# Optimization experiments

Hardware: AMD Instinct MI355X
Metric: run time of the kernel (lower is better)

The kernel has to match this reference:

```python
import math
import jax, jax.numpy as jnp
import numpy as np

# Module config (init_kwargs)
GRID = (11, 16, 24)          # (T, H, W) latent grid, T odd so T-1 == 2*(T//2)
POOL = 128                   # pool_size / block size
SPARSITY = 0.9
TXT_LEN = 384                # txt_len, txt_first=False
HEADS, HDIM = 8, 128
FFL = GRID[1] * GRID[2]      # first_frame_len = H*W = 384
SEQ = GRID[0] * FFL + TXT_LEN  # 4608 tokens, 36 blocks of 128


def _rearr(t):
    # rearrange_with_remaining, h%8==0 and w%8==0 path.
    # t: [b, (f h w), n, d] with f = T-1 frames (first frame excluded)
    b, s, n, d = t.shape
    T, H, W = GRID
    fn, hn, wn = T // 2, H // 8, W // 8
    x = t.transpose(0, 2, 1, 3).reshape(b * n, fn, 2, hn, 8, wn, 8, d)
    # 'b (fn fb)(hn hb)(wn wb) d -> b (fn hn wn fb hb wb) d'
    x = x.transpose(0, 1, 3, 5, 2, 4, 6, 7).reshape(b * n, s, d)
    return x.reshape(b, n, s, d).transpose(0, 2, 1, 3)


def _inv_rearr(t):
    b, s, n, d = t.shape
    T, H, W = GRID
    fn, hn, wn = T // 2, H // 8, W // 8
    x = t.transpose(0, 2, 1, 3).reshape(b * n, fn, hn, wn, 2, 8, 8, d)
    x = x.transpose(0, 1, 4, 2, 5, 3, 6, 7).reshape(b * n, s, d)
    return x.reshape(b, n, s, d).transpose(0, 2, 1, 3)


def _avgpool(t):
    # seq divisible by POOL -> mean over each block (tail branch unused)
    b, s, n, d = t.shape
    return t.reshape(b, s // POOL, POOL, n, d).mean(axis=2)


def _forward(q, k, v):
    b, s, n, d = q.shape
    scale = jnp.asarray(d, q.dtype) ** -0.5
    # do_tensor_rearrange_pooling on concatenated qkv (txt_first=False)
    qkv = jnp.concatenate([q, k, v], axis=0)
    f_part = qkv[:, :FFL]
    i_part = qkv[:, FFL:s - TXT_LEN]
    t_part = qkv[:, s - TXT_LEN:]
    qkv2 = jnp.concatenate([_rearr(i_part), f_part, t_part], axis=1)
    pool = _avgpool(qkv2)
    q2, k2, v2 = jnp.split(qkv2, 3, axis=0)
    qp, kp, _ = jnp.split(pool, 3, axis=0)
    # pooled block scores + softmax
    ps = jax.nn.softmax(jnp.einsum('blnd,bsnd->bnls', qp, kp) * scale, axis=-1)
    nb = s // POOL
    keep = math.ceil(nb * (1.0 - SPARSITY))
    thr = jax.lax.top_k(ps, keep)[0][..., -1:]
    mask = ps >= thr                              # [B, n, nb, nb] bool
    prot = (FFL + TXT_LEN + POOL - 1) // POOL
    mask = mask.at[:, :, -prot:, :].set(True)
    mask = mask.at[:, :, :, -prot:].set(True)
    bm = mask[0]                                  # [n, nb, nb] per-head block mask (batch 0, as kernel uses)
    tok = jnp.repeat(jnp.repeat(bm, POOL, axis=1), POOL, axis=2)  # [n, S, S]
    # block-sparse attention == masked dense attention over selected kv blocks
    scores = jnp.einsum('bqnd,bknd->bnqk', q2, k2) * scale
    scores = jnp.where(tok[None], scores, jnp.asarray(-1e30, scores.dtype))
    p = jax.nn.softmax(scores, axis=-1)
    x = jnp.einsum('bnqk,bknd->bqnd', p, v2)
    # do_tensor_inv_rearrange (txt_first=False: concat(f, i, t))
    si = s - TXT_LEN - FFL
    xi = _inv_rearr(x[:, :si])
    xf = x[:, si:si + FFL]
    xt = x[:, si + FFL:]
    return jnp.concatenate([xf, xi, xt], axis=1)


def setup_inputs() -> dict:
    key = jax.random.key(0)
    kq, kk, kv = jax.random.split(key, 3)
    q = jax.random.normal(kq, (1, SEQ, HEADS, HDIM), dtype=jnp.float32)
    k = jax.random.normal(kk, (1, SEQ, HEADS, HDIM), dtype=jnp.float32)
    v = jax.random.normal(kv, (1, SEQ, HEADS, HDIM), dtype=jnp.float32)
    t_b_idx = jnp.arange(2, dtype=jnp.int64 if jax.config.jax_enable_x64 else jnp.int32)
    return {'q': q, 'k': k, 'v': v, 't_b_idx': t_b_idx}


def reference(q, k, v, t_b_idx):
    # t_idx = t_b_idx[0] = 0, skip_timesteps = 0 -> sparse branch (static)
    return _forward(q, k, v)
```

## Files before the change

### kernel.cpp

```cpp
#include <hip/hip_runtime.h>


typedef __attribute__((ext_vector_type(8))) _Float16 half8;
typedef __attribute__((ext_vector_type(4))) _Float16 half4;
typedef __attribute__((ext_vector_type(2))) _Float16 half2v;
typedef __attribute__((ext_vector_type(4))) float float4v;

#define KROW 136
#define VROW 72
#define VSROW 138
#define PPROW 40

__device__ __forceinline__ int orig_pos(int j) {
    if (j >= 3840) return (j < 4224) ? (j - 3840) : j;
    int blk = j >> 7;
    int r   = j & 127;
    int f   = blk / 6;
    int rem = blk - f * 6;
    int b2  = rem / 3;
    int e   = rem - b2 * 3;
    int a   = r >> 6;
    int c   = (r >> 3) & 7;
    int g   = r & 7;
    return 384 + (f * 2 + a) * 384 + (b2 * 8 + c) * 24 + e * 8 + g;
}

__device__ __forceinline__ void cp16(const void* g, void* l) {
    __builtin_amdgcn_global_load_lds((const __attribute__((address_space(1))) void*)g,
                                     (__attribute__((address_space(3))) void*)l, 16, 0, 0);
}

__global__ __launch_bounds__(256) void conv_kernel(const float* __restrict__ k,
                                                   const float* __restrict__ v,
                                                   short* __restrict__ Kc,
                                                   unsigned* __restrict__ Vt32,
                                                   float* __restrict__ kpart) {
    __shared__ __align__(16) short KsL[64 * KROW];
    __shared__ short VsL[64 * VSROW];
    __shared__ float Rs[32 * 128];
    int bx  = blockIdx.x;
    int tid = threadIdx.x;
    int sub = bx & 1;
    int kb  = (bx >> 1) % 36;
    int h   = bx / 72;

    int lr  = tid >> 3;
    int ld4 = (tid & 7) << 2;

    float ksum[16];
#pragma unroll
    for (int i = 0; i < 16; ++i) ksum[i] = 0.f;

#pragma unroll
    for (int pass = 0; pass < 2; ++pass) {
        int lt  = pass * 32 + lr;
        int tok = sub * 64 + lt;
        int op  = orig_pos(kb * 128 + tok);
        const float* kr = k + ((size_t)op * 8 + h) * 128;
        const float* vr = v + ((size_t)op * 8 + h) * 128;
#pragma unroll
        for (int j = 0; j < 4; ++j) {
            int d = ld4 + j * 32;
            float4v xk = *reinterpret_cast<const float4v*>(kr + d);
            float4v xv = *reinterpret_cast<const float4v*>(vr + d);
            half4 hk;
            half2v hv0, hv1;
#pragma unroll
            for (int i = 0; i < 4; ++i) { hk[i] = (_Float16)xk[i]; ksum[j * 4 + i] += xk[i]; }
            hv0[0] = (_Float16)xv[0]; hv0[1] = (_Float16)xv[1];
            hv1[0] = (_Float16)xv[2]; hv1[1] = (_Float16)xv[3];
            *reinterpret_cast<half4*>(&KsL[lt * KROW + d]) = hk;
            *reinterpret_cast<half2v*>(&VsL[lt * VSROW + d]) = hv0;
            *reinterpret_cast<half2v*>(&VsL[lt * VSROW + d + 2]) = hv1;
        }
    }
#pragma unroll
    for (int j = 0; j < 4; ++j)
#pragma unroll
        for (int i = 0; i < 4; ++i)
            Rs[lr * 128 + ld4 + j * 32 + i] = ksum[j * 4 + i];
    __syncthreads();

    {
        const float4v* src = reinterpret_cast<const float4v*>(KsL);
        float4v* dst = reinterpret_cast<float4v*>(Kc + ((size_t)((h * 36 + kb) * 128) + sub * 64) * KROW);
        for (int i = tid; i < 1088; i += 256) dst[i] = src[i];
    }

    {
        const unsigned short* Vsu = (const unsigned short*)VsL;
        unsigned* vo = Vt32 + (size_t)((h * 36 + kb) * 2 + sub) * 128 * (VROW / 2);
#pragma unroll
        for (int it = 0; it < 16; ++it) {
            int i   = it * 256 + tid;
            int tw  = i & 31;
            int dim = i >> 5;
            unsigned lo = Vsu[(2 * tw) * VSROW + dim];
            unsigned hi = Vsu[(2 * tw + 1) * VSROW + dim];
            vo[dim * (VROW / 2) + tw] = (hi << 16) | lo;
        }
    }

    if (tid < 128) {
        float s = 0.f;
#pragma unroll
        for (int g = 0; g < 32; ++g) s += Rs[g * 128 + tid];
        kpart[(size_t)((h * 36 + kb) * 2 + sub) * 128 + tid] = s;
    }
}

__global__ __launch_bounds__(256) void poolq_kernel(const float* __restrict__ q,
                                                    float* __restrict__ qp) {
    __shared__ float Rs[8 * 128];
    int bx  = blockIdx.x;
    int tid = threadIdx.x;
    int kb  = bx % 36;
    int h   = bx / 36;

    int dq = (tid & 31) << 2;
    int g  = tid >> 5;
    float4v acc = {0.f, 0.f, 0.f, 0.f};
#pragma unroll
    for (int it = 0; it < 16; ++it) {
        int t  = g + it * 8;
        int op = orig_pos(kb * 128 + t);
        float4v x = *reinterpret_cast<const float4v*>(q + ((size_t)op * 8 + h) * 128 + dq);
        acc[0] += x[0]; acc[1] += x[1]; acc[2] += x[2]; acc[3] += x[3];
    }
#pragma unroll
    for (int i = 0; i < 4; ++i) Rs[g * 128 + dq + i] = acc[i];
    __syncthreads();

    if (tid < 128) {
        float s = 0.f;
#pragma unroll
        for (int g2 = 0; g2 < 8; ++g2) s += Rs[g2 * 128 + tid];
        qp[(h * 36 + kb) * 128 + tid] = s;
    }
}

__global__ __launch_bounds__(256, 3) void flash_kernel(const float* __restrict__ q,
                                                       const short* __restrict__ Kc,
                                                       const short* __restrict__ Vt,
                                                       const float* __restrict__ qp,
                                                       const float* __restrict__ kpart,
                                                       float* __restrict__ out,
                                                       float* __restrict__ pO,
                                                       float* __restrict__ pL) {
    __shared__ __align__(16) short Ks[64 * KROW];
    __shared__ __align__(16) short Vsh[128 * VROW];
    __shared__ __align__(16) short Ph[4 * 32 * PPROW];
    __shared__ int Ls[40];
    __shared__ float Lf[64];

    int t = blockIdx.x;
    int h, qb, half, nkb = 0, kbase = 0, pidx = -1;
    if (t < 288) {
        h = t & 7;
        int rest = t >> 3;
        int qbh = rest / 6, r2 = rest % 6;
        half = r2 / 3;
        int chunk = r2 % 3;
        qb = 30 + qbh; nkb = 12; kbase = chunk * 12; pidx = t;
    } else {
        int t2 = t - 288;
        h = t2 & 7;
        int rest = t2 >> 3;
        qb = rest >> 1; half = rest & 1;
    }

    int tid = threadIdx.x, wave = tid >> 6, lane = tid & 63;
    int m16 = lane & 15, quad = lane >> 4;
    int rh = wave & 1, th = wave >> 1;

    constexpr float kScale = 0.08838834764831845f * 1.4426950408889634f;

    half8 aq[2][4];
#pragma unroll
    for (int rg = 0; rg < 2; ++rg) {
        int qrow_frag = qb * 128 + half * 64 + rh * 32 + rg * 16 + m16;
        const float* qrp = q + ((size_t)orig_pos(qrow_frag) * 8 + h) * 128;
#pragma unroll
        for (int kc = 0; kc < 4; ++kc) {
            float4v x0 = *reinterpret_cast<const float4v*>(qrp + kc * 32 + quad * 8);
            float4v x1 = *reinterpret_cast<const float4v*>(qrp + kc * 32 + quad * 8 + 4);
#pragma unroll
            for (int j = 0; j < 4; ++j) {
                aq[rg][kc][j]     = (_Float16)(x0[j] * kScale);
                aq[rg][kc][4 + j] = (_Float16)(x1[j] * kScale);
            }
        }
    }

    if (pidx < 0 && wave == 0) {
        float s = -1e30f;
        if (lane < 36) {
            const float4v* qv  = (const float4v*)(qp + (h * 36 + qb) * 128);
            const float4v* kv0 = (const float4v*)(kpart + (size_t)((h * 36 + lane) * 2) * 128);
            const float4v* kv1 = kv0 + 32;
            float acc = 0.f;
            for (int i = 0; i < 32; ++i) {
                float4v a = qv[i], b0 = kv0[i], b1 = kv1[i];
                acc += a[0] * (b0[0] + b1[0]) + a[1] * (b0[1] + b1[1])
                     + a[2] * (b0[2] + b1[2]) + a[3] * (b0[3] + b1[3]);
            }
            s = acc;
        }
        float tmp = s;
        float thr = 0.f;
        for (int i = 0; i < 4; ++i) {
            float mx = tmp;
            for (int off = 1; off < 64; off <<= 1) mx = fmaxf(mx, __shfl_xor(mx, off));
            thr = mx;
            unsigned long long bal = __ballot(tmp == mx);
            int low = __ffsll(bal) - 1;
            if (lane == low) tmp = -3e38f;
        }
        bool keep = (lane < 36) && ((s >= thr) || (lane >= 30));
        unsigned long long mk = __ballot(keep);
        if (lane == 0) Ls[0] = __popcll(mk);
        if (keep) {
            int pos = __popcll(mk & ((1ull << lane) - 1ull));
            Ls[1 + pos] = lane;
        }
    }
    __syncthreads();
    if (pidx < 0) nkb = Ls[0];

    float l_r[2][4];
    float4v o[2][8];
#pragma unroll
    for (int rg = 0; rg < 2; ++rg) {
#pragma unroll
        for (int r = 0; r < 4; ++r) l_r[rg][r] = 0.f;
#pragma unroll
        for (int dt = 0; dt < 8; ++dt) { o[rg][dt][0] = 0.f; o[rg][dt][1] = 0.f; o[rg][dt][2] = 0.f; o[rg][dt][3] = 0.f; }
    }

    short* Phw = Ph + wave * (32 * PPROW);

    int ntile = nkb * 2;
    for (int it = 0; it < ntile; ++it) {
        int kb  = (pidx >= 0) ? (kbase + (it >> 1)) : Ls[1 + (it >> 1)];
        int sub = it & 1;
        const char* gK = (const char*)(Kc + ((size_t)((h * 36 + kb) * 128) + sub * 64) * KROW);
        const char* gV = (const char*)(Vt + (size_t)((h * 36 + kb) * 2 + sub) * 128 * VROW);

        __syncthreads();
        {
            char* lK = (char*)Ks;
            char* lV = (char*)Vsh;
            int off = lane * 16;
            for (int c = wave; c < 35; c += 4) {
                if (c < 17) cp16(gK + c * 1024 + off, lK + c * 1024 + off);
                else        cp16(gV + (c - 17) * 1024 + off, lV + (c - 17) * 1024 + off);
            }
        }
        __syncthreads();

        float4v sacc[2][2];
#pragma unroll
        for (int rg = 0; rg < 2; ++rg)
#pragma unroll
            for (int nt = 0; nt < 2; ++nt) { sacc[rg][nt][0] = 0.f; sacc[rg][nt][1] = 0.f; sacc[rg][nt][2] = 0.f; sacc[rg][nt][3] = 0.f; }
#pragma unroll
        for (int nt = 0; nt < 2; ++nt)
#pragma unroll
            for (int kc = 0; kc < 4; ++kc) {
                half8 bk = *reinterpret_cast<const half8*>(&Ks[(th * 32 + nt * 16 + m16) * KROW + kc * 32 + quad * 8]);
                sacc[0][nt] = __builtin_amdgcn_mfma_f32_16x16x32_f16(aq[0][kc], bk, sacc[0][nt], 0, 0, 0);
                sacc[1][nt] = __builtin_amdgcn_mfma_f32_16x16x32_f16(aq[1][kc], bk, sacc[1][nt], 0, 0, 0);
            }

#pragma unroll
        for (int rg = 0; rg < 2; ++rg)
#pragma unroll
            for (int r = 0; r < 4; ++r) {
                float p0 = exp2f(sacc[rg][0][r]);
                float p1 = exp2f(sacc[rg][1][r]);
                sacc[rg][0][r] = p0; sacc[rg][1][r] = p1;
                l_r[rg][r] += p0 + p1;
            }

#pragma unroll
        for (int rg = 0; rg < 2; ++rg)
#pragma unroll
            for (int nt = 0; nt < 2; ++nt)
#pragma unroll
                for (int r = 0; r < 4; ++r) {
                    union { _Float16 hf; short s; } cv;
                    cv.hf = (_Float16)sacc[rg][nt][r];
                    Phw[(rg * 16 + quad * 4 + r) * PPROW + nt * 16 + m16] = cv.s;
                }
        half8 ap[2];
#pragma unroll
        for (int rg = 0; rg < 2; ++rg)
            ap[rg] = *reinterpret_cast<const half8*>(&Phw[(rg * 16 + m16) * PPROW + quad * 8]);

#pragma unroll
        for (int dt = 0; dt < 8; ++dt) {
            half8 bv = *reinterpret_cast<const half8*>(&Vsh[(dt * 16 + m16) * VROW + th * 32 + quad * 8]);
            o[0][dt] = __builtin_amdgcn_mfma_f32_16x16x32_f16(ap[0], bv, o[0][dt], 0, 0, 0);
            o[1][dt] = __builtin_amdgcn_mfma_f32_16x16x32_f16(ap[1], bv, o[1][dt], 0, 0, 0);
        }
    }

#pragma unroll
    for (int rg = 0; rg < 2; ++rg)
#pragma unroll
        for (int r = 0; r < 4; ++r)
            for (int sh = 1; sh < 16; sh <<= 1) l_r[rg][r] += __shfl_xor(l_r[rg][r], sh);

    __syncthreads();
    {
        float* red = rh ? (float*)Vsh : (float*)Ks;
        if (th == 1) {
#pragma unroll
            for (int rg = 0; rg < 2; ++rg) {
#pragma unroll
                for (int dt = 0; dt < 8; ++dt)
#pragma unroll
                    for (int r = 0; r < 4; ++r)
                        red[(rg * 16 + quad * 4 + r) * 132 + dt * 16 + m16] = o[rg][dt][r];
                if (m16 == 0)
#pragma unroll
                    for (int r = 0; r < 4; ++r)
                        Lf[rh * 32 + rg * 16 + quad * 4 + r] = l_r[rg][r];
            }
        }
        __syncthreads();
        if (th == 0) {
#pragma unroll
            for (int rg = 0; rg < 2; ++rg)
#pragma unroll
                for (int dt = 0; dt < 8; ++dt)
#pragma unroll
                    for (int r = 0; r < 4; ++r)
                        o[rg][dt][r] += red[(rg * 16 + quad * 4 + r) * 132 + dt * 16 + m16];

            if (pidx >= 0) {
                float* po = pO + (size_t)pidx * 8192;
#pragma unroll
                for (int rg = 0; rg < 2; ++rg)
#pragma unroll
                    for (int r = 0; r < 4; ++r) {
                        int row = rh * 32 + rg * 16 + quad * 4 + r;
                        float lt2 = l_r[rg][r] + Lf[row];
#pragma unroll
                        for (int dt = 0; dt < 8; ++dt)
                            po[row * 128 + dt * 16 + m16] = o[rg][dt][r];
                        if (m16 == 0) pL[pidx * 64 + row] = lt2;
                    }
            } else {
#pragma unroll
                for (int rg = 0; rg < 2; ++rg)
#pragma unroll
                    for (int r = 0; r < 4; ++r) {
                        int row = rh * 32 + rg * 16 + quad * 4 + r;
                        int qrow = qb * 128 + half * 64 + row;
                        size_t base = ((size_t)orig_pos(qrow) * 8 + h) * 128;
                        float inv = 1.f / (l_r[rg][r] + Lf[row]);
#pragma unroll
                        for (int dt = 0; dt < 8; ++dt)
                            out[base + dt * 16 + m16] = o[rg][dt][r] * inv;
                    }
            }
        }
    }
}

__global__ void combine_kernel(const float* __restrict__ pO, const float* __restrict__ pL,
                               float* __restrict__ out) {
    int gb = blockIdx.x;
    int g  = gb >> 3;
    int rg = gb & 7;
    int h    = g / 12;
    int rem  = g % 12;
    int qbh  = rem >> 1;
    int half = rem & 1;
    int qb   = 30 + qbh;
    int base_t = (qbh * 6 + half * 3) * 8 + h;

    int tid = threadIdx.x;
    int d   = tid & 127;
    int r0  = tid >> 7;
#pragma unroll
    for (int itr = 0; itr < 4; ++itr) {
        int row = rg * 8 + r0 + itr * 2;
        float l = pL[(base_t + 0) * 64 + row] + pL[(base_t + 8) * 64 + row] + pL[(base_t + 16) * 64 + row];
        float acc = pO[(size_t)(base_t + 0) * 8192 + row * 128 + d]
                  + pO[(size_t)(base_t + 8) * 8192 + row * 128 + d]
                  + pO[(size_t)(base_t + 16) * 8192 + row * 128 + d];
        int qrow = qb * 128 + half * 64 + row;
        out[((size_t)orig_pos(qrow) * 8 + h) * 128 + d] = acc / l;
    }
}

extern "C" void kernel_launch(void* const* d_in, const int* in_sizes, int n_in,
                              void* d_out, int out_size, void* d_ws, size_t ws_size,
                              hipStream_t stream) {
    const float* q = (const float*)d_in[0];
    const float* k = (const float*)d_in[1];
    const float* v = (const float*)d_in[2];
    float* out = (float*)d_out;

    char* w = (char*)d_ws;
    short* Kc    = (short*)(w);
    short* Vt    = (short*)(w + 10027008);
    float* qp    = (float*)(w + 20643840);
    float* kpart = (float*)(w + 20791296);
    float* pL    = (float*)(w + 21086208);
    float* pO    = (float*)(w + 21159936);

    conv_kernel<<<dim3(576), dim3(256), 0, stream>>>(k, v, Kc, (unsigned*)Vt, kpart);
    poolq_kernel<<<dim3(288), dim3(256), 0, stream>>>(q, qp);
    flash_kernel<<<dim3(768), dim3(256), 0, stream>>>(q, Kc, Vt, qp, kpart, out, pO, pL);
    combine_kernel<<<dim3(768), dim3(256), 0, stream>>>(pO, pL, out);
}
```

Baseline: 172.4 us.

## Merge prep kernels and fold split-K combine into flash via atomic tickets

Merges the K/V conversion and Q pooling kernels into a single prep launch. It also removes the separate combine kernel: each split-K flash block takes an atomic ticket, and the last of the three blocks in a group reduces the partial outputs and writes the final result. This removes two kernel launches and the gaps between them. In exchange, the reduction runs serialized inside one block per group, and correctness depends on threadfence ordering and on the ticket array being zeroed in the prep kernel.

```diff
diff --git a/kernel.cpp b/kernel.cpp
--- a/kernel.cpp
+++ b/kernel.cpp
@@ -30,112 +30,115 @@
                                      (__attribute__((address_space(3))) void*)l, 16, 0, 0);
 }
 
-__global__ __launch_bounds__(256) void conv_kernel(const float* __restrict__ k,
+__global__ __launch_bounds__(256) void prep_kernel(const float* __restrict__ q,
+                                                   const float* __restrict__ k,
                                                    const float* __restrict__ v,
                                                    short* __restrict__ Kc,
                                                    unsigned* __restrict__ Vt32,
-                                                   float* __restrict__ kpart) {
+                                                   float* __restrict__ qp,
+                                                   float* __restrict__ kpart,
+                                                   int* __restrict__ tickets) {
     __shared__ __align__(16) short KsL[64 * KROW];
     __shared__ short VsL[64 * VSROW];
     __shared__ float Rs[32 * 128];
     int bx  = blockIdx.x;
     int tid = threadIdx.x;
-    int sub = bx & 1;
-    int kb  = (bx >> 1) % 36;
-    int h   = bx / 72;
-
-    int lr  = tid >> 3;
-    int ld4 = (tid & 7) << 2;
-
-    float ksum[16];
-#pragma unroll
-    for (int i = 0; i < 16; ++i) ksum[i] = 0.f;
-
-#pragma unroll
-    for (int pass = 0; pass < 2; ++pass) {
-        int lt  = pass * 32 + lr;
-        int tok = sub * 64 + lt;
-        int op  = orig_pos(kb * 128 + tok);
-        const float* kr = k + ((size_t)op * 8 + h) * 128;
-        const float* vr = v + ((size_t)op * 8 + h) * 128;
-#pragma unroll
-        for (int j = 0; j < 4; ++j) {
-            int d = ld4 + j * 32;
-            float4v xk = *reinterpret_cast<const float4v*>(kr + d);
-            float4v xv = *reinterpret_cast<const float4v*>(vr + d);
-            half4 hk;
-            half2v hv0, hv1;
-#pragma unroll
-            for (int i = 0; i < 4; ++i) { hk[i] = (_Float16)xk[i]; ksum[j * 4 + i] += xk[i]; }
-            hv0[0] = (_Float16)xv[0]; hv0[1] = (_Float16)xv[1];
-            hv1[0] = (_Float16)xv[2]; hv1[1] = (_Float16)xv[3];
-            *reinterpret_cast<half4*>(&KsL[lt * KROW + d]) = hk;
-            *reinterpret_cast<half2v*>(&VsL[lt * VSROW + d]) = hv0;
-            *reinterpret_cast<half2v*>(&VsL[lt * VSROW + d + 2]) = hv1;
-        }
-    }
-#pragma unroll
-    for (int j = 0; j < 4; ++j)
-#pragma unroll
-        for (int i = 0; i < 4; ++i)
-            Rs[lr * 128 + ld4 + j * 32 + i] = ksum[j * 4 + i];
-    __syncthreads();
-
-    {
-        const float4v* src = reinterpret_cast<const float4v*>(KsL);
-        float4v* dst = reinterpret_cast<float4v*>(Kc + ((size_t)((h * 36 + kb) * 128) + sub * 64) * KROW);
-        for (int i = tid; i < 1088; i += 256) dst[i] = src[i];
-    }
-
-    {
-        const unsigned short* Vsu = (const unsigned short*)VsL;
-        unsigned* vo = Vt32 + (size_t)((h * 36 + kb) * 2 + sub) * 128 * (VROW / 2);
+
+    if (bx < 576) {
+        int sub = bx & 1;
+        int kb  = (bx >> 1) % 36;
+        int h   = bx / 72;
+
+        int lr  = tid >> 3;
+        int ld4 = (tid & 7) << 2;
+
+        float ksum[16];
+#pragma unroll
+        for (int i = 0; i < 16; ++i) ksum[i] = 0.f;
+
+#pragma unroll
+        for (int pass = 0; pass < 2; ++pass) {
+            int lt  = pass * 32 + lr;
+            int tok = sub * 64 + lt;
+            int op  = orig_pos(kb * 128 + tok);
+            const float* kr = k + ((size_t)op * 8 + h) * 128;
+            const float* vr = v + ((size_t)op * 8 + h) * 128;
+#pragma unroll
+            for (int j = 0; j < 4; ++j) {
+                int d = ld4 + j * 32;
+                float4v xk = *reinterpret_cast<const float4v*>(kr + d);
+                float4v xv = *reinterpret_cast<const float4v*>(vr + d);
+                half4 hk;
+                half2v hv0, hv1;
+#pragma unroll
+                for (int i = 0; i < 4; ++i) { hk[i] = (_Float16)xk[i]; ksum[j * 4 + i] += xk[i]; }
+                hv0[0] = (_Float16)xv[0]; hv0[1] = (_Float16)xv[1];
+                hv1[0] = (_Float16)xv[2]; hv1[1] = (_Float16)xv[3];
+                *reinterpret_cast<half4*>(&KsL[lt * KROW + d]) = hk;
+                *reinterpret_cast<half2v*>(&VsL[lt * VSROW + d]) = hv0;
+                *reinterpret_cast<half2v*>(&VsL[lt * VSROW + d + 2]) = hv1;
+            }
+        }
+#pragma unroll
+        for (int j = 0; j < 4; ++j)
+#pragma unroll
+            for (int i = 0; i < 4; ++i)
+                Rs[lr * 128 + ld4 + j * 32 + i] = ksum[j * 4 + i];
+        __syncthreads();
+
+        {
+            const float4v* src = reinterpret_cast<const float4v*>(KsL);
+            float4v* dst = reinterpret_cast<float4v*>(Kc + ((size_t)((h * 36 + kb) * 128) + sub * 64) * KROW);
+            for (int i = tid; i < 1088; i += 256) dst[i] = src[i];
+        }
+
+        {
+            const unsigned short* Vsu = (const unsigned short*)VsL;
+            unsigned* vo = Vt32 + (size_t)((h * 36 + kb) * 2 + sub) * 128 * (VROW / 2);
+#pragma unroll
+            for (int it = 0; it < 16; ++it) {
+                int i   = it * 256 + tid;
+                int tw  = i & 31;
+                int dim = i >> 5;
+                unsigned lo = Vsu[(2 * tw) * VSROW + dim];
+                unsigned hi = Vsu[(2 * tw + 1) * VSROW + dim];
+                vo[dim * (VROW / 2) + tw] = (hi << 16) | lo;
+            }
+        }
+
+        if (tid < 128) {
+            float s = 0.f;
+#pragma unroll
+            for (int g = 0; g < 32; ++g) s += Rs[g * 128 + tid];
+            kpart[(size_t)((h * 36 + kb) * 2 + sub) * 128 + tid] = s;
+        }
+    } else {
+        int bx2 = bx - 576;
+        int kb  = bx2 % 36;
+        int h   = bx2 / 36;
+
+        if (bx2 == 0 && tid < 96) tickets[tid] = 0;
+
+        int dq = (tid & 31) << 2;
+        int g  = tid >> 5;
+        float4v acc = {0.f, 0.f, 0.f, 0.f};
 #pragma unroll
         for (int it = 0; it < 16; ++it) {
-            int i   = it * 256 + tid;
-            int tw  = i & 31;
-            int dim = i >> 5;
-            unsigned lo = Vsu[(2 * tw) * VSROW + dim];
-            unsigned hi = Vsu[(2 * tw + 1) * VSROW + dim];
-            vo[dim * (VROW / 2) + tw] = (hi << 16) | lo;
-        }
-    }
-
-    if (tid < 128) {
-        float s = 0.f;
-#pragma unroll
-        for (int g = 0; g < 32; ++g) s += Rs[g * 128 + tid];
-        kpart[(size_t)((h * 36 + kb) * 2 + sub) * 128 + tid] = s;
-    }
-}
-
-__global__ __launch_bounds__(256) void poolq_kernel(const float* __restrict__ q,
-                                                    float* __restrict__ qp) {
-    __shared__ float Rs[8 * 128];
-    int bx  = blockIdx.x;
-    int tid = threadIdx.x;
-    int kb  = bx % 36;
-    int h   = bx / 36;
-
-    int dq = (tid & 31) << 2;
-    int g  = tid >> 5;
-    float4v acc = {0.f, 0.f, 0.f, 0.f};
-#pragma unroll
-    for (int it = 0; it < 16; ++it) {
-        int t  = g + it * 8;
-        int op = orig_pos(kb * 128 + t);
-        float4v x = *reinterpret_cast<const float4v*>(q + ((size_t)op * 8 + h) * 128 + dq);
-        acc[0] += x[0]; acc[1] += x[1]; acc[2] += x[2]; acc[3] += x[3];
-    }
-#pragma unroll
-    for (int i = 0; i < 4; ++i) Rs[g * 128 + dq + i] = acc[i];
-    __syncthreads();
-
-    if (tid < 128) {
-        float s = 0.f;
-#pragma unroll
-        for (int g2 = 0; g2 < 8; ++g2) s += Rs[g2 * 128 + tid];
-        qp[(h * 36 + kb) * 128 + tid] = s;
+            int t  = g + it * 8;
+            int op = orig_pos(kb * 128 + t);
+            float4v x = *reinterpret_cast<const float4v*>(q + ((size_t)op * 8 + h) * 128 + dq);
+            acc[0] += x[0]; acc[1] += x[1]; acc[2] += x[2]; acc[3] += x[3];
+        }
+#pragma unroll
+        for (int i = 0; i < 4; ++i) Rs[g * 128 + dq + i] = acc[i];
+        __syncthreads();
+
+        if (tid < 128) {
+            float s = 0.f;
+#pragma unroll
+            for (int g2 = 0; g2 < 8; ++g2) s += Rs[g2 * 128 + tid];
+            qp[(h * 36 + kb) * 128 + tid] = s;
+        }
     }
 }
 
@@ -146,7 +149,8 @@
                                                        const float* __restrict__ kpart,
                                                        float* __restrict__ out,
                                                        float* __restrict__ pO,
-                                                       float* __restrict__ pL) {
+                                                       float* __restrict__ pL,
+                                                       int* __restrict__ tickets) {
     __shared__ __align__(16) short Ks[64 * KROW];
     __shared__ __align__(16) short Vsh[128 * VROW];
     __shared__ __align__(16) short Ph[4 * 32 * PPROW];
@@ -154,11 +158,12 @@
     __shared__ float Lf[64];
 
     int t = blockIdx.x;
-    int h, qb, half, nkb = 0, kbase = 0, pidx = -1;
+    int h, qb, half, nkb = 0, kbase = 0, pidx = -1, qbh = 0;
     if (t < 288) {
         h = t & 7;
         int rest = t >> 3;
-        int qbh = rest / 6, r2 = rest % 6;
+        qbh = rest / 6;
+        int r2 = rest % 6;
         half = r2 / 3;
         int chunk = r2 % 3;
         qb = 30 + qbh; nkb = 12; kbase = chunk * 12; pidx = t;
@@ -367,32 +372,29 @@
             }
         }
     }
-}
-
-__global__ void combine_kernel(const float* __restrict__ pO, const float* __restrict__ pL,
-                               float* __restrict__ out) {
-    int gb = blockIdx.x;
-    int g  = gb >> 3;
-    int rg = gb & 7;
-    int h    = g / 12;
-    int rem  = g % 12;
-    int qbh  = rem >> 1;
-    int half = rem & 1;
-    int qb   = 30 + qbh;
-    int base_t = (qbh * 6 + half * 3) * 8 + h;
-
-    int tid = threadIdx.x;
-    int d   = tid & 127;
-    int r0  = tid >> 7;
-#pragma unroll
-    for (int itr = 0; itr < 4; ++itr) {
-        int row = rg * 8 + r0 + itr * 2;
-        float l = pL[(base_t + 0) * 64 + row] + pL[(base_t + 8) * 64 + row] + pL[(base_t + 16) * 64 + row];
-        float acc = pO[(size_t)(base_t + 0) * 8192 + row * 128 + d]
-                  + pO[(size_t)(base_t + 8) * 8192 + row * 128 + d]
-                  + pO[(size_t)(base_t + 16) * 8192 + row * 128 + d];
-        int qrow = qb * 128 + half * 64 + row;
-        out[((size_t)orig_pos(qrow) * 8 + h) * 128 + d] = acc / l;
+
+    if (pidx >= 0) {
+        int grp = h * 12 + qbh * 2 + half;
+        __threadfence();
+        __syncthreads();
+        if (tid == 0) Ls[39] = atomicAdd(&tickets[grp], 1);
+        __syncthreads();
+        if (Ls[39] == 2) {
+            __threadfence();
+            int base_t = (qbh * 6 + half * 3) * 8 + h;
+            int d  = tid & 127;
+            int r0 = tid >> 7;
+#pragma unroll 4
+            for (int itr = 0; itr < 32; ++itr) {
+                int row = r0 + itr * 2;
+                float l = pL[(base_t + 0) * 64 + row] + pL[(base_t + 8) * 64 + row] + pL[(base_t + 16) * 64 + row];
+                float acc = pO[(size_t)(base_t + 0) * 8192 + row * 128 + d]
+                          + pO[(size_t)(base_t + 8) * 8192 + row * 128 + d]
+                          + pO[(size_t)(base_t + 16) * 8192 + row * 128 + d];
+                int qrow = qb * 128 + half * 64 + row;
+                out[((size_t)orig_pos(qrow) * 8 + h) * 128 + d] = acc / l;
+            }
+        }
     }
 }
 
@@ -411,9 +413,8 @@
     float* kpart = (float*)(w + 20791296);
     float* pL    = (float*)(w + 21086208);
     float* pO    = (float*)(w + 21159936);
-
-    conv_kernel<<<dim3(576), dim3(256), 0, stream>>>(k, v, Kc, (unsigned*)Vt, kpart);
-    poolq_kernel<<<dim3(288), dim3(256), 0, stream>>>(q, qp);
-    flash_kernel<<<dim3(768), dim3(256), 0, stream>>>(q, Kc, Vt, qp, kpart, out, pO, pL);
-    combine_kernel<<<dim3(768), dim3(256), 0, stream>>>(pO, pL, out);
+    int*   tick  = (int*)(w + 30597120);
+
+    prep_kernel<<<dim3(864), dim3(256), 0, stream>>>(q, k, v, Kc, (unsigned*)Vt, qp, kpart, tick);
+    flash_kernel<<<dim3(768), dim3(256), 0, stream>>>(q, Kc, Vt, qp, kpart, out, pO, pL, tick);
 }
```

Measured after the change: 215.3 us. 24.8% more time.

## Merge prep kernels, split heavy query blocks four ways, reuse K LDS for P

Applied to the files above, without the earlier changes.

Merges the K/V conversion and Q pooling kernels into one launch. The dense protected query blocks are now split into four KV chunks of 9 blocks instead of three of 12, and the grid is remapped to 864 blocks that interleave heavy and light work items. The P staging buffer now aliases the K shared tile, which needs an extra barrier per tile but frees LDS, and launch bounds are raised to 4 blocks per SM. The aim is better load balance and occupancy plus one fewer launch, at the cost of an extra sync and more partial outputs for the combine step to read.

```diff
diff --git a/kernel.cpp b/kernel.cpp
--- a/kernel.cpp
+++ b/kernel.cpp
@@ -30,116 +30,116 @@
                                      (__attribute__((address_space(3))) void*)l, 16, 0, 0);
 }
 
-__global__ __launch_bounds__(256) void conv_kernel(const float* __restrict__ k,
+__global__ __launch_bounds__(256) void prep_kernel(const float* __restrict__ q,
+                                                   const float* __restrict__ k,
                                                    const float* __restrict__ v,
                                                    short* __restrict__ Kc,
                                                    unsigned* __restrict__ Vt32,
+                                                   float* __restrict__ qp,
                                                    float* __restrict__ kpart) {
     __shared__ __align__(16) short KsL[64 * KROW];
     __shared__ short VsL[64 * VSROW];
     __shared__ float Rs[32 * 128];
     int bx  = blockIdx.x;
     int tid = threadIdx.x;
-    int sub = bx & 1;
-    int kb  = (bx >> 1) % 36;
-    int h   = bx / 72;
-
-    int lr  = tid >> 3;
-    int ld4 = (tid & 7) << 2;
-
-    float ksum[16];
-#pragma unroll
-    for (int i = 0; i < 16; ++i) ksum[i] = 0.f;
-
-#pragma unroll
-    for (int pass = 0; pass < 2; ++pass) {
-        int lt  = pass * 32 + lr;
-        int tok = sub * 64 + lt;
-        int op  = orig_pos(kb * 128 + tok);
-        const float* kr = k + ((size_t)op * 8 + h) * 128;
-        const float* vr = v + ((size_t)op * 8 + h) * 128;
-#pragma unroll
-        for (int j = 0; j < 4; ++j) {
-            int d = ld4 + j * 32;
-            float4v xk = *reinterpret_cast<const float4v*>(kr + d);
-            float4v xv = *reinterpret_cast<const float4v*>(vr + d);
-            half4 hk;
-            half2v hv0, hv1;
-#pragma unroll
-            for (int i = 0; i < 4; ++i) { hk[i] = (_Float16)xk[i]; ksum[j * 4 + i] += xk[i]; }
-            hv0[0] = (_Float16)xv[0]; hv0[1] = (_Float16)xv[1];
-            hv1[0] = (_Float16)xv[2]; hv1[1] = (_Float16)xv[3];
-            *reinterpret_cast<half4*>(&KsL[lt * KROW + d]) = hk;
-            *reinterpret_cast<half2v*>(&VsL[lt * VSROW + d]) = hv0;
-            *reinterpret_cast<half2v*>(&VsL[lt * VSROW + d + 2]) = hv1;
-        }
-    }
-#pragma unroll
-    for (int j = 0; j < 4; ++j)
-#pragma unroll
-        for (int i = 0; i < 4; ++i)
-            Rs[lr * 128 + ld4 + j * 32 + i] = ksum[j * 4 + i];
-    __syncthreads();
-
-    {
-        const float4v* src = reinterpret_cast<const float4v*>(KsL);
-        float4v* dst = reinterpret_cast<float4v*>(Kc + ((size_t)((h * 36 + kb) * 128) + sub * 64) * KROW);
-        for (int i = tid; i < 1088; i += 256) dst[i] = src[i];
-    }
-
-    {
-        const unsigned short* Vsu = (const unsigned short*)VsL;
-        unsigned* vo = Vt32 + (size_t)((h * 36 + kb) * 2 + sub) * 128 * (VROW / 2);
+
+    if (bx < 576) {
+        int sub = bx & 1;
+        int kb  = (bx >> 1) % 36;
+        int h   = bx / 72;
+
+        int lr  = tid >> 3;
+        int ld4 = (tid & 7) << 2;
+
+        float ksum[16];
+#pragma unroll
+        for (int i = 0; i < 16; ++i) ksum[i] = 0.f;
+
+#pragma unroll
+        for (int pass = 0; pass < 2; ++pass) {
+            int lt  = pass * 32 + lr;
+            int tok = sub * 64 + lt;
+            int op  = orig_pos(kb * 128 + tok);
+            const float* kr = k + ((size_t)op * 8 + h) * 128;
+            const float* vr = v + ((size_t)op * 8 + h) * 128;
+#pragma unroll
+            for (int j = 0; j < 4; ++j) {
+                int d = ld4 + j * 32;
+                float4v xk = *reinterpret_cast<const float4v*>(kr + d);
+                float4v xv = *reinterpret_cast<const float4v*>(vr + d);
+                half4 hk;
+                half2v hv0, hv1;
+#pragma unroll
+                for (int i = 0; i < 4; ++i) { hk[i] = (_Float16)xk[i]; ksum[j * 4 + i] += xk[i]; }
+                hv0[0] = (_Float16)xv[0]; hv0[1] = (_Float16)xv[1];
+                hv1[0] = (_Float16)xv[2]; hv1[1] = (_Float16)xv[3];
+                *reinterpret_cast<half4*>(&KsL[lt * KROW + d]) = hk;
+                *reinterpret_cast<half2v*>(&VsL[lt * VSROW + d]) = hv0;
+                *reinterpret_cast<half2v*>(&VsL[lt * VSROW + d + 2]) = hv1;
+            }
+        }
+#pragma unroll
+        for (int j = 0; j < 4; ++j)
+#pragma unroll
+            for (int i = 0; i < 4; ++i)
+                Rs[lr * 128 + ld4 + j * 32 + i] = ksum[j * 4 + i];
+        __syncthreads();
+
+        {
+            const float4v* src = reinterpret_cast<const float4v*>(KsL);
+            float4v* dst = reinterpret_cast<float4v*>(Kc + ((size_t)((h * 36 + kb) * 128) + sub * 64) * KROW);
+            for (int i = tid; i < 1088; i += 256) dst[i] = src[i];
+        }
+
+        {
+            const unsigned short* Vsu = (const unsigned short*)VsL;
+            unsigned* vo = Vt32 + (size_t)((h * 36 + kb) * 2 + sub) * 128 * (VROW / 2);
+#pragma unroll
+            for (int it = 0; it < 16; ++it) {
+                int i   = it * 256 + tid;
+                int tw  = i & 31;
+                int dim = i >> 5;
+                unsigned lo = Vsu[(2 * tw) * VSROW + dim];
+                unsigned hi = Vsu[(2 * tw + 1) * VSROW + dim];
+                vo[dim * (VROW / 2) + tw] = (hi << 16) | lo;
+            }
+        }
+
+        if (tid < 128) {
+            float s = 0.f;
+#pragma unroll
+            for (int g = 0; g < 32; ++g) s += Rs[g * 128 + tid];
+            kpart[(size_t)((h * 36 + kb) * 2 + sub) * 128 + tid] = s;
+        }
+    } else {
+        int bx2 = bx - 576;
+        int kb  = bx2 % 36;
+        int h   = bx2 / 36;
+
+        int dq = (tid & 31) << 2;
+        int g  = tid >> 5;
+        float4v acc = {0.f, 0.f, 0.f, 0.f};
 #pragma unroll
         for (int it = 0; it < 16; ++it) {
-            int i   = it * 256 + tid;
-            int tw  = i & 31;
-            int dim = i >> 5;
-            unsigned lo = Vsu[(2 * tw) * VSROW + dim];
-            unsigned hi = Vsu[(2 * tw + 1) * VSROW + dim];
-            vo[dim * (VROW / 2) + tw] = (hi << 16) | lo;
-        }
-    }
-
-    if (tid < 128) {
-        float s = 0.f;
-#pragma unroll
-        for (int g = 0; g < 32; ++g) s += Rs[g * 128 + tid];
-        kpart[(size_t)((h * 36 + kb) * 2 + sub) * 128 + tid] = s;
-    }
-}
-
-__global__ __launch_bounds__(256) void poolq_kernel(const float* __restrict__ q,
-                                                    float* __restrict__ qp) {
-    __shared__ float Rs[8 * 128];
-    int bx  = blockIdx.x;
-    int tid = threadIdx.x;
-    int kb  = bx % 36;
-    int h   = bx / 36;
-
-    int dq = (tid & 31) << 2;
-    int g  = tid >> 5;
-    float4v acc = {0.f, 0.f, 0.f, 0.f};
-#pragma unroll
-    for (int it = 0; it < 16; ++it) {
-        int t  = g + it * 8;
-        int op = orig_pos(kb * 128 + t);
-        float4v x = *reinterpret_cast<const float4v*>(q + ((size_t)op * 8 + h) * 128 + dq);
-        acc[0] += x[0]; acc[1] += x[1]; acc[2] += x[2]; acc[3] += x[3];
-    }
-#pragma unroll
-    for (int i = 0; i < 4; ++i) Rs[g * 128 + dq + i] = acc[i];
-    __syncthreads();
-
-    if (tid < 128) {
-        float s = 0.f;
-#pragma unroll
-        for (int g2 = 0; g2 < 8; ++g2) s += Rs[g2 * 128 + tid];
-        qp[(h * 36 + kb) * 128 + tid] = s;
-    }
-}
-
-__global__ __launch_bounds__(256, 3) void flash_kernel(const float* __restrict__ q,
+            int t  = g + it * 8;
+            int op = orig_pos(kb * 128 + t);
+            float4v x = *reinterpret_cast<const float4v*>(q + ((size_t)op * 8 + h) * 128 + dq);
+            acc[0] += x[0]; acc[1] += x[1]; acc[2] += x[2]; acc[3] += x[3];
+        }
+#pragma unroll
+        for (int i = 0; i < 4; ++i) Rs[g * 128 + dq + i] = acc[i];
+        __syncthreads();
+
+        if (tid < 128) {
+            float s = 0.f;
+#pragma unroll
+            for (int g2 = 0; g2 < 8; ++g2) s += Rs[g2 * 128 + tid];
+            qp[(h * 36 + kb) * 128 + tid] = s;
+        }
+    }
+}
+
+__global__ __launch_bounds__(256, 4) void flash_kernel(const float* __restrict__ q,
                                                        const short* __restrict__ Kc,
                                                        const short* __restrict__ Vt,
                                                        const float* __restrict__ qp,
@@ -149,24 +149,27 @@
                                                        float* __restrict__ pL) {
     __shared__ __align__(16) short Ks[64 * KROW];
     __shared__ __align__(16) short Vsh[128 * VROW];
-    __shared__ __align__(16) short Ph[4 * 32 * PPROW];
     __shared__ int Ls[40];
     __shared__ float Lf[64];
 
-    int t = blockIdx.x;
-    int h, qb, half, nkb = 0, kbase = 0, pidx = -1;
-    if (t < 288) {
-        h = t & 7;
-        int rest = t >> 3;
-        int qbh = rest / 6, r2 = rest % 6;
-        half = r2 / 3;
-        int chunk = r2 % 3;
-        qb = 30 + qbh; nkb = 12; kbase = chunk * 12; pidx = t;
-    } else {
-        int t2 = t - 288;
-        h = t2 & 7;
-        int rest = t2 >> 3;
-        qb = rest >> 1; half = rest & 1;
+    int b = blockIdx.x;
+    int c = b & 255, s = b >> 8;
+    int h = c & 7, u = c >> 3;
+    int qb, half, nkb = 0, kbase = 0, pidx = -1, qbh = 0;
+    {
+        bool heavy; int j, jl;
+        if (u < 12)      { heavy = (s == 0); j = u;                  jl = u * 3 + (s - 1); }
+        else if (u < 28) { heavy = (s <= 1); j = 12 + (u - 12) * 2 + s; jl = 36 + (u - 12); }
+        else             { heavy = (s == 0); j = 44 + (u - 28);      jl = 52 + (u - 28) * 2 + (s - 1); }
+        if (heavy) {
+            qbh = j >> 3;
+            int r = j & 7;
+            half = r >> 2;
+            int chunk = r & 3;
+            qb = 30 + qbh; nkb = 9; kbase = chunk * 9; pidx = h * 48 + j;
+        } else {
+            qb = jl >> 1; half = jl & 1;
+        }
     }
 
     int tid = threadIdx.x, wave = tid >> 6, lane = tid & 63;
@@ -185,15 +188,15 @@
             float4v x0 = *reinterpret_cast<const float4v*>(qrp + kc * 32 + quad * 8);
             float4v x1 = *reinterpret_cast<const float4v*>(qrp + kc * 32 + quad * 8 + 4);
 #pragma unroll
-            for (int j = 0; j < 4; ++j) {
-                aq[rg][kc][j]     = (_Float16)(x0[j] * kScale);
-                aq[rg][kc][4 + j] = (_Float16)(x1[j] * kScale);
+            for (int j2 = 0; j2 < 4; ++j2) {
+                aq[rg][kc][j2]     = (_Float16)(x0[j2] * kScale);
+                aq[rg][kc][4 + j2] = (_Float16)(x1[j2] * kScale);
             }
         }
     }
 
     if (pidx < 0 && wave == 0) {
-        float s = -1e30f;
+        float sc = -1e30f;
         if (lane < 36) {
             const float4v* qv  = (const float4v*)(qp + (h * 36 + qb) * 128);
             const float4v* kv0 = (const float4v*)(kpart + (size_t)((h * 36 + lane) * 2) * 128);
@@ -204,9 +207,9 @@
                 acc += a[0] * (b0[0] + b1[0]) + a[1] * (b0[1] + b1[1])
                      + a[2] * (b0[2] + b1[2]) + a[3] * (b0[3] + b1[3]);
             }
-            s = acc;
-        }
-        float tmp = s;
+            sc = acc;
+        }
+        float tmp = sc;
         float thr = 0.f;
         for (int i = 0; i < 4; ++i) {
             float mx = tmp;
@@ -216,7 +219,7 @@
             int low = __ffsll(bal) - 1;
             if (lane == low) tmp = -3e38f;
         }
-        bool keep = (lane < 36) && ((s >= thr) || (lane >= 30));
+        bool keep = (lane < 36) && ((sc >= thr) || (lane >= 30));
         unsigned long long mk = __ballot(keep);
         if (lane == 0) Ls[0] = __popcll(mk);
         if (keep) {
@@ -237,7 +240,7 @@
         for (int dt = 0; dt < 8; ++dt) { o[rg][dt][0] = 0.f; o[rg][dt][1] = 0.f; o[rg][dt][2] = 0.f; o[rg][dt][3] = 0.f; }
     }
 
-    short* Phw = Ph + wave * (32 * PPROW);
+    short* Phw = ((short*)Ks) + wave * (32 * PPROW);
 
     int ntile = nkb * 2;
     for (int it = 0; it < ntile; ++it) {
@@ -251,9 +254,9 @@
             char* lK = (char*)Ks;
             char* lV = (char*)Vsh;
             int off = lane * 16;
-            for (int c = wave; c < 35; c += 4) {
-                if (c < 17) cp16(gK + c * 1024 + off, lK + c * 1024 + off);
-                else        cp16(gV + (c - 17) * 1024 + off, lV + (c - 17) * 1024 + off);
+            for (int ch = wave; ch < 35; ch += 4) {
+                if (ch < 17) cp16(gK + ch * 1024 + off, lK + ch * 1024 + off);
+                else         cp16(gV + (ch - 17) * 1024 + off, lV + (ch - 17) * 1024 + off);
             }
         }
         __syncthreads();
@@ -282,15 +285,17 @@
                 l_r[rg][r] += p0 + p1;
             }
 
+        __syncthreads();
+
 #pragma unroll
         for (int rg = 0; rg < 2; ++rg)
 #pragma unroll
             for (int nt = 0; nt < 2; ++nt)
 #pragma unroll
                 for (int r = 0; r < 4; ++r) {
-                    union { _Float16 hf; short s; } cv;
+                    union { _Float16 hf; short sv; } cv;
                     cv.hf = (_Float16)sacc[rg][nt][r];
-                    Phw[(rg * 16 + quad * 4 + r) * PPROW + nt * 16 + m16] = cv.s;
+                    Phw[(rg * 16 + quad * 4 + r) * PPROW + nt * 16 + m16] = cv.sv;
                 }
         half8 ap[2];
 #pragma unroll
@@ -372,14 +377,14 @@
 __global__ void combine_kernel(const float* __restrict__ pO, const float* __restrict__ pL,
                                float* __restrict__ out) {
     int gb = blockIdx.x;
-    int g  = gb >> 3;
-    int rg = gb & 7;
-    int h    = g / 12;
-    int rem  = g % 12;
+    int gid = gb >> 3;
+    int rg  = gb & 7;
+    int h    = gid / 12;
+    int rem  = gid % 12;
     int qbh  = rem >> 1;
     int half = rem & 1;
     int qb   = 30 + qbh;
-    int base_t = (qbh * 6 + half * 3) * 8 + h;
+    int p0   = h * 48 + qbh * 8 + half * 4;
 
     int tid = threadIdx.x;
     int d   = tid & 127;
@@ -387,10 +392,12 @@
 #pragma unroll
     for (int itr = 0; itr < 4; ++itr) {
         int row = rg * 8 + r0 + itr * 2;
-        float l = pL[(base_t + 0) * 64 + row] + pL[(base_t + 8) * 64 + row] + pL[(base_t + 16) * 64 + row];
-        float acc = pO[(size_t)(base_t + 0) * 8192 + row * 128 + d]
-                  + pO[(size_t)(base_t + 8) * 8192 + row * 128 + d]
-                  + pO[(size_t)(base_t + 16) * 8192 + row * 128 + d];
+        float l = pL[(p0 + 0) * 64 + row] + pL[(p0 + 1) * 64 + row]
+                + pL[(p0 + 2) * 64 + row] + pL[(p0 + 3) * 64 + row];
+        float acc = pO[(size_t)(p0 + 0) * 8192 + row * 128 + d]
+                  + pO[(size_t)(p0 + 1) * 8192 + row * 128 + d]
+                  + pO[(size_t)(p0 + 2) * 8192 + row * 128 + d]
+                  + pO[(size_t)(p0 + 3) * 8192 + row * 128 + d];
         int qrow = qb * 128 + half * 64 + row;
         out[((size_t)orig_pos(qrow) * 8 + h) * 128 + d] = acc / l;
     }
@@ -410,10 +417,9 @@
     float* qp    = (float*)(w + 20643840);
     float* kpart = (float*)(w + 20791296);
     float* pL    = (float*)(w + 21086208);
-    float* pO    = (float*)(w + 21159936);
-
-    conv_kernel<<<dim3(576), dim3(256), 0, stream>>>(k, v, Kc, (unsigned*)Vt, kpart);
-    poolq_kernel<<<dim3(288), dim3(256), 0, stream>>>(q, qp);
-    flash_kernel<<<dim3(768), dim3(256), 0, stream>>>(q, Kc, Vt, qp, kpart, out, pO, pL);
+    float* pO    = (float*)(w + 21184512);
+
+    prep_kernel<<<dim3(864), dim3(256), 0, stream>>>(q, k, v, Kc, (unsigned*)Vt, qp, kpart);
+    flash_kernel<<<dim3(864), dim3(256), 0, stream>>>(q, Kc, Vt, qp, kpart, out, pO, pL);
     combine_kernel<<<dim3(768), dim3(256), 0, stream>>>(pO, pL, out);
 }
```

New measurement: 269.6 us. +56.4%, slower.
